# Optimization experiments

Hardware: AMD Instinct MI355X
Metric: run time of the kernel (lower is better)

The kernel has to match this reference:

```python
import jax, jax.numpy as jnp
import numpy as np

B, T, D, VQ, L2, HID = 8, 2048, 768, 64, 12, 1024
K = 2 ** L2          # 4096 codebook entries
N_MID = 4            # condition_layer=6 -> 1 input + 4 middle + 1 output Linear, 5 BatchNorms
EPS_N = 1e-6
EPS_BN = 1e-5


def setup_inputs() -> dict:
    key = jax.random.key(0)
    ks = jax.random.split(key, 10)
    g = lambda i, shape, sc: jax.random.normal(ks[i], shape, jnp.float32) * sc
    return {
        "h_in": jax.random.normal(ks[0], (B, D, T), jnp.float32),
        "attn_mask": jax.random.randint(ks[1], (B, T), 0, 2, jnp.int32),
        "proj_w": g(2, (VQ, D), 0.02), "proj_b": jnp.zeros((VQ,), jnp.float32),
        "inv_w": g(3, (D, VQ), 0.02), "inv_b": jnp.zeros((D,), jnp.float32),
        "mlp_w_in": g(4, (HID, L2), 0.1), "mlp_b_in": jnp.zeros((HID,), jnp.float32),
        "mlp_w_mid": g(5, (N_MID, HID, HID), 0.03), "mlp_b_mid": jnp.zeros((N_MID, HID), jnp.float32),
        "mlp_w_out": g(6, (VQ, HID), 0.03), "mlp_b_out": jnp.zeros((VQ,), jnp.float32),
        "bn_gamma": jnp.ones((N_MID + 1, HID), jnp.float32),
        "bn_beta": jnp.zeros((N_MID + 1, HID), jnp.float32),
    }


def _bn(x, gamma, beta):
    # BatchNorm1d, training mode: batch mean / biased var over codebook rows
    m = x.mean(axis=0)
    v = x.var(axis=0)
    return (x - m) * jax.lax.rsqrt(v + EPS_BN) * gamma + beta


def _l2norm(x):
    return x / (jnp.linalg.norm(x, axis=-1, keepdims=True) + EPS_N)


def reference(h_in, attn_mask, proj_w, proj_b, inv_w, inv_b,
              mlp_w_in, mlp_b_in, mlp_w_mid, mlp_b_mid, mlp_w_out, mlp_b_out,
              bn_gamma, bn_beta):
    # --- codebook: binary vectors -> condition MLP (Linear+BN+ReLU x5, Linear) ---
    ints = jnp.arange(K)
    bits = ((ints[:, None] & (1 << jnp.arange(L2 - 1, -1, -1))) > 0).astype(jnp.float32)  # [K, L2]
    x = jax.nn.relu(_bn(bits @ mlp_w_in.T + mlp_b_in, bn_gamma[0], bn_beta[0]))
    for i in range(N_MID):
        x = jax.nn.relu(_bn(x @ mlp_w_mid[i].T + mlp_b_mid[i], bn_gamma[i + 1], bn_beta[i + 1]))
    embed = x @ mlp_w_out.T + mlp_b_out          # [K, VQ]
    embed = _l2norm(embed)                        # sphere=True

    # --- project hidden states: h_in [B,D,T] -> [B,T,VQ] ---
    h = jnp.einsum('bdt,vd->btv', h_in, proj_w) + proj_b
    h = _l2norm(h)

    # --- pairwise squared distances to codebook, argmax of -d (== softmax argmax) ---
    hf = h.reshape(-1, VQ)                                       # [B*T, VQ]
    d = (hf ** 2).sum(-1, keepdims=True) + (embed ** 2).sum(-1) - 2.0 * (hf @ embed.T)  # [B*T, K]
    code = jnp.argmax(-d, axis=-1)                               # [B*T]

    # --- masked gather/scatter quantization (eval path: hard codes) ---
    mask = (attn_mask == 1)                                      # [B, T]
    h_vq = embed[code].reshape(B, T, VQ) * mask[..., None].astype(h.dtype)
    quantized = jnp.einsum('btv,dv->btd', h_vq, inv_w) + inv_b   # proj_inv -> [B, T, D]
    vq_code = jnp.where(mask, code.reshape(B, T), 0)
    return quantized, vq_code
```

## Files before the change

kernel.cpp:

```cpp
#include <hip/hip_runtime.h>
#include <stddef.h>

#define BB   8
#define TT_  2048
#define DD   768
#define VQ_  64
#define L2C  12
#define HID_ 1024
#define KK   4096
#define NMID 4
#define NT   (BB*TT_)

typedef _Float16 h8v __attribute__((ext_vector_type(8)));
typedef float    f4v __attribute__((ext_vector_type(4)));

#define LDA 40

__global__ __launch_bounds__(256) void k_mlp_in(const float* __restrict__ w_in,
                                                const float* __restrict__ b_in,
                                                float* __restrict__ X) {
    __shared__ float ws_[256 * 12];
    __shared__ float bs_[256];
    int tid = threadIdx.x;
    int h0  = blockIdx.x * 256;
    for (int i = tid; i < 256 * 12; i += 256) ws_[i] = w_in[h0 * 12 + i];
    bs_[tid] = b_in[h0 + tid];
    __syncthreads();
    float w[12];
#pragma unroll
    for (int l = 0; l < 12; l++) w[l] = ws_[tid * 12 + l];
    float bias = bs_[tid];
    int k0 = blockIdx.y * 16;
    for (int kk = 0; kk < 16; kk++) {
        int k = k0 + kk;
        float acc = bias;
#pragma unroll
        for (int l = 0; l < 12; l++)
            if ((k >> (11 - l)) & 1) acc += w[l];
        X[(size_t)k * HID_ + h0 + tid] = acc;
    }
}

__global__ __launch_bounds__(256) void k_bn_stats1(const float* __restrict__ Y,
                                                   float* __restrict__ part) {
    int b = blockIdx.x, t = threadIdx.x;
    const float* src = Y + ((size_t)b << 6) * HID_ + (t << 2);
    float sx = 0.f, sy = 0.f, sz = 0.f, sw = 0.f;
    float qx = 0.f, qy = 0.f, qz = 0.f, qw = 0.f;
    for (int r = 0; r < 64; r++) {
        float4 v = *(const float4*)(src + ((size_t)r << 10));
        sx += v.x; sy += v.y; sz += v.z; sw += v.w;
        qx += v.x * v.x; qy += v.y * v.y; qz += v.z * v.z; qw += v.w * v.w;
    }
    *(float4*)(part + ((size_t)b << 10) + (t << 2)) = make_float4(sx, sy, sz, sw);
    *(float4*)(part + 65536 + ((size_t)b << 10) + (t << 2)) = make_float4(qx, qy, qz, qw);
}

__global__ __launch_bounds__(256) void k_bn_stats2(const float* __restrict__ part,
                                                   float* __restrict__ mv) {
    int c = blockIdx.x * 256 + threadIdx.x;
    float s = 0.f, q = 0.f;
    for (int b = 0; b < 64; b++) {
        s += part[((size_t)b << 10) + c];
        q += part[65536 + ((size_t)b << 10) + c];
    }
    float m = s * (1.f / KK);
    float v = q * (1.f / KK) - m * m;
    mv[c] = m; mv[HID_ + c] = v;
}

__global__ __launch_bounds__(256) void k_bn_apply_split(const float* __restrict__ Y,
                                                        const float* __restrict__ mv,
                                                        const float* __restrict__ gamma,
                                                        const float* __restrict__ beta,
                                                        _Float16* __restrict__ Xhi,
                                                        _Float16* __restrict__ Xlo) {
    int i = blockIdx.x * 256 + threadIdx.x;
    int c = (i << 2) & (HID_ - 1);
    float4 x = ((const float4*)Y)[i];
    float4 m = *(const float4*)(mv + c);
    float4 v = *(const float4*)(mv + HID_ + c);
    float4 g = *(const float4*)(gamma + c);
    float4 b = *(const float4*)(beta + c);
    float o[4];
    o[0] = fmaxf(0.f, (x.x - m.x) * (1.f / sqrtf(v.x + 1e-5f)) * g.x + b.x);
    o[1] = fmaxf(0.f, (x.y - m.y) * (1.f / sqrtf(v.y + 1e-5f)) * g.y + b.y);
    o[2] = fmaxf(0.f, (x.z - m.z) * (1.f / sqrtf(v.z + 1e-5f)) * g.z + b.z);
    o[3] = fmaxf(0.f, (x.w - m.w) * (1.f / sqrtf(v.w + 1e-5f)) * g.w + b.w);
    union { _Float16 h[4]; uint2 u; } uh, ul;
#pragma unroll
    for (int j = 0; j < 4; j++) {
        _Float16 h = (_Float16)o[j];
        uh.h[j] = h;
        ul.h[j] = (_Float16)(o[j] - (float)h);
    }
    *(uint2*)(Xhi + ((size_t)i << 2)) = uh.u;
    *(uint2*)(Xlo + ((size_t)i << 2)) = ul.u;
}

__global__ __launch_bounds__(256) void k_gemm_mfma(const _Float16* __restrict__ Ahi,
                                                   const _Float16* __restrict__ Alo,
                                                   const float* __restrict__ W,
                                                   const float* __restrict__ bias,
                                                   float* __restrict__ C,
                                                   int M, int N, int Kd) {
    __shared__ _Float16 sAh[128 * LDA];
    __shared__ _Float16 sAl[128 * LDA];
    __shared__ _Float16 sWh[64 * LDA];
    __shared__ _Float16 sWl[64 * LDA];
    const int tid = threadIdx.x;
    const int m0 = blockIdx.x * 128, n0 = blockIdx.y * 64;
    const int wave = tid >> 6, lane = tid & 63;
    const int wm = (wave >> 1) << 6;
    const int wn = (wave & 1) << 5;
    const int l15 = lane & 15, quad = lane >> 4;

    const int ar = tid >> 1;
    const int ak = (tid & 1) << 4;
    const int wr = tid >> 2;
    const int wk = (tid & 3) << 3;

    f4v acc[4][2];
#pragma unroll
    for (int i = 0; i < 4; i++)
#pragma unroll
        for (int j = 0; j < 2; j++) acc[i][j] = (f4v){0.f, 0.f, 0.f, 0.f};

    const size_t abase = (size_t)(m0 + ar) * Kd + ak;
    const size_t wbase = (size_t)(n0 + wr) * Kd + wk;

    for (int k0 = 0; k0 < Kd; k0 += 32) {
        uint4 a0 = *(const uint4*)(Ahi + abase + k0);
        uint4 a1 = *(const uint4*)(Ahi + abase + k0 + 8);
        uint4 c0 = *(const uint4*)(Alo + abase + k0);
        uint4 c1 = *(const uint4*)(Alo + abase + k0 + 8);
        float4 w0 = *(const float4*)(W + wbase + k0);
        float4 w1 = *(const float4*)(W + wbase + k0 + 4);
        union { _Float16 h[8]; uint4 u; } wh, wl;
        float wf[8] = {w0.x, w0.y, w0.z, w0.w, w1.x, w1.y, w1.z, w1.w};
#pragma unroll
        for (int j = 0; j < 8; j++) {
            _Float16 h = (_Float16)wf[j];
            wh.h[j] = h;
            wl.h[j] = (_Float16)(wf[j] - (float)h);
        }
        __syncthreads();
        *(uint4*)(sAh + ar * LDA + ak)     = a0;
        *(uint4*)(sAh + ar * LDA + ak + 8) = a1;
        *(uint4*)(sAl + ar * LDA + ak)     = c0;
        *(uint4*)(sAl + ar * LDA + ak + 8) = c1;
        *(uint4*)(sWh + wr * LDA + wk) = wh.u;
        *(uint4*)(sWl + wr * LDA + wk) = wl.u;
        __syncthreads();

        h8v ah[4], alv[4], bh[2], bl[2];
#pragma unroll
        for (int i = 0; i < 4; i++) {
            ah[i]  = *(const h8v*)(sAh + (wm + (i << 4) + l15) * LDA + (quad << 3));
            alv[i] = *(const h8v*)(sAl + (wm + (i << 4) + l15) * LDA + (quad << 3));
        }
#pragma unroll
        for (int j = 0; j < 2; j++) {
            bh[j] = *(const h8v*)(sWh + (wn + (j << 4) + l15) * LDA + (quad << 3));
            bl[j] = *(const h8v*)(sWl + (wn + (j << 4) + l15) * LDA + (quad << 3));
        }
#pragma unroll
        for (int i = 0; i < 4; i++)
#pragma unroll
            for (int j = 0; j < 2; j++) {
                acc[i][j] = __builtin_amdgcn_mfma_f32_16x16x32_f16(ah[i],  bh[j], acc[i][j], 0, 0, 0);
                acc[i][j] = __builtin_amdgcn_mfma_f32_16x16x32_f16(ah[i],  bl[j], acc[i][j], 0, 0, 0);
                acc[i][j] = __builtin_amdgcn_mfma_f32_16x16x32_f16(alv[i], bh[j], acc[i][j], 0, 0, 0);
            }
    }
#pragma unroll
    for (int j = 0; j < 2; j++) {
        int col = n0 + wn + (j << 4) + l15;
        float bv = bias[col];
#pragma unroll
        for (int i = 0; i < 4; i++) {
            int row = m0 + wm + (i << 4) + (quad << 2);
#pragma unroll
            for (int r = 0; r < 4; r++)
                C[(size_t)(row + r) * N + col] = acc[i][j][r] + bv;
        }
    }
}

__global__ __launch_bounds__(256) void k_l2norm(float* __restrict__ E,
                                                float* __restrict__ eqh,
                                                _Float16* __restrict__ Ehi,
                                                _Float16* __restrict__ Elo) {
    int tid = threadIdx.x;
    int row = blockIdx.x * 4 + (tid >> 6);
    int v = tid & 63;
    size_t off = ((size_t)row << 6) + v;
    float x = E[off];
    float ss = x * x;
#pragma unroll
    for (int o = 32; o; o >>= 1) ss += __shfl_xor(ss, o, 64);
    float inv = 1.f / (sqrtf(ss) + 1e-6f);
    float xn = x * inv;
    E[off] = xn;
    _Float16 hh = (_Float16)xn;
    Ehi[off] = hh;
    Elo[off] = (_Float16)(xn - (float)hh);
    if (v == 0) eqh[row] = -0.5f * (ss * inv * inv);
}

__global__ __launch_bounds__(256) void k_wsplit(const float* __restrict__ pw,
                                                _Float16* __restrict__ pwhi,
                                                _Float16* __restrict__ pwlo) {
    int i = blockIdx.x * 256 + threadIdx.x;
    float4 w = ((const float4*)pw)[i];
    float wf[4] = {w.x, w.y, w.z, w.w};
    union { _Float16 h[4]; uint2 u; } uh, ul;
#pragma unroll
    for (int j = 0; j < 4; j++) {
        _Float16 h = (_Float16)wf[j];
        uh.h[j] = h;
        ul.h[j] = (_Float16)(wf[j] - (float)h);
    }
    *(uint2*)(pwhi + ((size_t)i << 2)) = uh.u;
    *(uint2*)(pwlo + ((size_t)i << 2)) = ul.u;
}

__global__ __launch_bounds__(256) void k_proj_mfma(const float* __restrict__ h_in,
                                                   const _Float16* __restrict__ pwhi,
                                                   const _Float16* __restrict__ pwlo,
                                                   float* __restrict__ Hpart) {
    __shared__ float shA[128 * 33];
    const int tid = threadIdx.x;
    const int t0 = blockIdx.x * 128;
    const int ks = blockIdx.y;
    const int b = t0 >> 11;
    const int tloc0 = t0 & (TT_ - 1);
    const int wave = tid >> 6, lane = tid & 63;
    const int l15 = lane & 15, quad = lane >> 4;

    const int dl = tid >> 3;
    const int tg = (tid & 7) << 4;

    f4v acc[2][4];
#pragma unroll
    for (int i = 0; i < 2; i++)
#pragma unroll
        for (int j = 0; j < 4; j++) acc[i][j] = (f4v){0.f, 0.f, 0.f, 0.f};

    for (int kk = 0; kk < 6; kk++) {
        int dd0 = ks * 192 + kk * 32;
        const float* src = h_in + ((size_t)(b * DD + dd0 + dl) << 11) + tloc0 + tg;
        float4 g0 = *(const float4*)(src);
        float4 g1 = *(const float4*)(src + 4);
        float4 g2 = *(const float4*)(src + 8);
        float4 g3 = *(const float4*)(src + 12);
        __syncthreads();
        float gv[16] = {g0.x, g0.y, g0.z, g0.w, g1.x, g1.y, g1.z, g1.w,
                        g2.x, g2.y, g2.z, g2.w, g3.x, g3.y, g3.z, g3.w};
#pragma unroll
        for (int i = 0; i < 16; i++) shA[(tg + i) * 33 + dl] = gv[i];
        __syncthreads();

        h8v ah[2], al[2];
#pragma unroll
        for (int mt = 0; mt < 2; mt++) {
            const float* ap = &shA[((wave << 5) + (mt << 4) + l15) * 33 + (quad << 3)];
            float4 a0 = *(const float4*)(ap);
            float4 a1 = *(const float4*)(ap + 4);
            float av[8] = {a0.x, a0.y, a0.z, a0.w, a1.x, a1.y, a1.z, a1.w};
#pragma unroll
            for (int j = 0; j < 8; j++) {
                _Float16 h = (_Float16)av[j];
                ah[mt][j] = h;
                al[mt][j] = (_Float16)(av[j] - (float)h);
            }
        }
#pragma unroll
        for (int nt = 0; nt < 4; nt++) {
            size_t wb = (size_t)((nt << 4) + l15) * DD + dd0 + (quad << 3);
            h8v bh = *(const h8v*)(pwhi + wb);
            h8v bl = *(const h8v*)(pwlo + wb);
#pragma unroll
            for (int mt = 0; mt < 2; mt++) {
                acc[mt][nt] = __builtin_amdgcn_mfma_f32_16x16x32_f16(ah[mt], bh, acc[mt][nt], 0, 0, 0);
                acc[mt][nt] = __builtin_amdgcn_mfma_f32_16x16x32_f16(ah[mt], bl, acc[mt][nt], 0, 0, 0);
                acc[mt][nt] = __builtin_amdgcn_mfma_f32_16x16x32_f16(al[mt], bh, acc[mt][nt], 0, 0, 0);
            }
        }
    }
    float* dst = Hpart + ((size_t)ks << 20);
#pragma unroll
    for (int mt = 0; mt < 2; mt++) {
#pragma unroll
        for (int r = 0; r < 4; r++) {
            int t = t0 + (wave << 5) + (mt << 4) + (quad << 2) + r;
#pragma unroll
            for (int nt = 0; nt < 4; nt++)
                dst[((size_t)t << 6) + (nt << 4) + l15] = acc[mt][nt][r];
        }
    }
}

__global__ __launch_bounds__(256) void k_hnorm(const float* __restrict__ Hpart,
                                               const float* __restrict__ pb,
                                               _Float16* __restrict__ Hhi,
                                               _Float16* __restrict__ Hlo) {
    __shared__ float ssp[4][64];
    int tid = threadIdx.x;
    int tt = tid & 63, vg = tid >> 6;
    int t = blockIdx.x * 64 + tt;
    size_t base = ((size_t)t << 6) + (vg << 4);
    float o[16];
#pragma unroll
    for (int u = 0; u < 4; u++) {
        float4 p0 = *(const float4*)(Hpart + (0u << 20) + base + (u << 2));
        float4 p1 = *(const float4*)(Hpart + (1u << 20) + base + (u << 2));
        float4 p2 = *(const float4*)(Hpart + (2u << 20) + base + (u << 2));
        float4 p3 = *(const float4*)(Hpart + (3u << 20) + base + (u << 2));
        o[u * 4 + 0] = p0.x + p1.x + p2.x + p3.x;
        o[u * 4 + 1] = p0.y + p1.y + p2.y + p3.y;
        o[u * 4 + 2] = p0.z + p1.z + p2.z + p3.z;
        o[u * 4 + 3] = p0.w + p1.w + p2.w + p3.w;
    }
    float sp = 0.f;
#pragma unroll
    for (int j = 0; j < 16; j++) {
        o[j] += pb[(vg << 4) + j];
        sp = fmaf(o[j], o[j], sp);
    }
    ssp[vg][tt] = sp;
    __syncthreads();
    float ss = ssp[0][tt] + ssp[1][tt] + ssp[2][tt] + ssp[3][tt];
    float inv = 1.f / (sqrtf(ss) + 1e-6f);
    union { _Float16 h[8]; uint4 u; } uh0, uh1, ul0, ul1;
#pragma unroll
    for (int j = 0; j < 16; j++) {
        float xn = o[j] * inv;
        _Float16 hh = (_Float16)xn;
        _Float16 ll = (_Float16)(xn - (float)hh);
        if (j < 8) { uh0.h[j] = hh; ul0.h[j] = ll; }
        else       { uh1.h[j - 8] = hh; ul1.h[j - 8] = ll; }
    }
    *(uint4*)(Hhi + base)     = uh0.u;
    *(uint4*)(Hhi + base + 8) = uh1.u;
    *(uint4*)(Hlo + base)     = ul0.u;
    *(uint4*)(Hlo + base + 8) = ul1.u;
}

__global__ __launch_bounds__(256) void k_argmax_mfma(const _Float16* __restrict__ Hhi,
                                                     const _Float16* __restrict__ Hlo,
                                                     const _Float16* __restrict__ Ehi,
                                                     const _Float16* __restrict__ Elo,
                                                     const float* __restrict__ eqh,
                                                     float* __restrict__ ps,
                                                     int* __restrict__ pi) {
    int tid = threadIdx.x;
    int wave = tid >> 6, lane = tid & 63;
    int l15 = lane & 15, quad = lane >> 4;
    int t0 = blockIdx.x * 256 + wave * 64;
    int kh = blockIdx.y;
    const int kbase = kh << 9;

    h8v hh0[4], hh1[4], hl0[4], hl1[4];
#pragma unroll
    for (int s = 0; s < 4; s++) {
        size_t hb = (size_t)(t0 + (s << 4) + l15) * 64 + (quad << 3);
        hh0[s] = *(const h8v*)(Hhi + hb);
        hh1[s] = *(const h8v*)(Hhi + hb + 32);
        hl0[s] = *(const h8v*)(Hlo + hb);
        hl1[s] = *(const h8v*)(Hlo + hb + 32);
    }
    float best[4] = {-1e30f, -1e30f, -1e30f, -1e30f};
    int   idx[4]  = {0, 0, 0, 0};

    size_t eb = (size_t)(kbase + l15) * 64 + (quad << 3);
    h8v eh0 = *(const h8v*)(Ehi + eb);
    h8v eh1 = *(const h8v*)(Ehi + eb + 32);
    h8v el0 = *(const h8v*)(Elo + eb);
    h8v el1 = *(const h8v*)(Elo + eb + 32);
    float4 q4 = *(const float4*)(eqh + kbase + (quad << 2));

    for (int it = 0; it < 32; it++) {
        h8v ce0 = eh0, ce1 = eh1, cl0 = el0, cl1 = el1;
        float4 cq = q4;
        int k0 = kbase + (it << 4);
        int kn = k0 + 16;
        if (kn > KK - 16) kn = KK - 16;
        size_t ebn = (size_t)(kn + l15) * 64 + (quad << 3);
        eh0 = *(const h8v*)(Ehi + ebn);
        eh1 = *(const h8v*)(Ehi + ebn + 32);
        el0 = *(const h8v*)(Elo + ebn);
        el1 = *(const h8v*)(Elo + ebn + 32);
        q4 = *(const float4*)(eqh + kn + (quad << 2));

        f4v acc[4];
#pragma unroll
        for (int s = 0; s < 4; s++) acc[s] = (f4v){0.f, 0.f, 0.f, 0.f};
#pragma unroll
        for (int s = 0; s < 4; s++) acc[s] = __builtin_amdgcn_mfma_f32_16x16x32_f16(ce0, hh0[s], acc[s], 0, 0, 0);
#pragma unroll
        for (int s = 0; s < 4; s++) acc[s] = __builtin_amdgcn_mfma_f32_16x16x32_f16(ce1, hh1[s], acc[s], 0, 0, 0);
#pragma unroll
        for (int s = 0; s < 4; s++) acc[s] = __builtin_amdgcn_mfma_f32_16x16x32_f16(cl0, hh0[s], acc[s], 0, 0, 0);
#pragma unroll
        for (int s = 0; s < 4; s++) acc[s] = __builtin_amdgcn_mfma_f32_16x16x32_f16(cl1, hh1[s], acc[s], 0, 0, 0);
#pragma unroll
        for (int s = 0; s < 4; s++) acc[s] = __builtin_amdgcn_mfma_f32_16x16x32_f16(ce0, hl0[s], acc[s], 0, 0, 0);
#pragma unroll
        for (int s = 0; s < 4; s++) acc[s] = __builtin_amdgcn_mfma_f32_16x16x32_f16(ce1, hl1[s], acc[s], 0, 0, 0);
        float qv[4] = {cq.x, cq.y, cq.z, cq.w};
#pragma unroll
        for (int r = 0; r < 4; r++) {
            int k = k0 + (quad << 2) + r;
#pragma unroll
            for (int s = 0; s < 4; s++) {
                float sc = acc[s][r] + qv[r];
                if (sc > best[s]) { best[s] = sc; idx[s] = k; }
            }
        }
    }
#pragma unroll
    for (int m = 16; m <= 32; m <<= 1) {
#pragma unroll
        for (int s = 0; s < 4; s++) {
            float ob = __shfl_xor(best[s], m, 64);
            int   oi = __shfl_xor(idx[s], m, 64);
            if (ob > best[s] || (ob == best[s] && oi < idx[s])) { best[s] = ob; idx[s] = oi; }
        }
    }
    if (quad == 0) {
#pragma unroll
        for (int s = 0; s < 4; s++) {
            int t = t0 + (s << 4) + l15;
            ps[(size_t)t * 8 + kh] = best[s];
            pi[(size_t)t * 8 + kh] = idx[s];
        }
    }
}

__global__ __launch_bounds__(256) void k_merge(const float* __restrict__ ps,
                                               const int* __restrict__ pi,
                                               const int* __restrict__ mask,
                                               const float* __restrict__ E,
                                               float* __restrict__ G,
                                               float* __restrict__ outc) {
    __shared__ int codes[256];
    __shared__ int ms[256];
    int tid = threadIdx.x;
    int base = blockIdx.x << 8;
    int t = base + tid;
    float best = ps[(size_t)t * 8];
    int bi = pi[(size_t)t * 8];
#pragma unroll
    for (int s = 1; s < 8; s++) {
        float v = ps[(size_t)t * 8 + s];
        if (v > best) { best = v; bi = pi[(size_t)t * 8 + s]; }
    }
    int m = mask[t];
    codes[tid] = bi;
    ms[tid] = m;
    outc[t] = m ? (float)bi : 0.0f;
    __syncthreads();
    for (int i = tid; i < 256 * 16; i += 256) {
        int r = i >> 4, u = i & 15;
        float4 e = ms[r] ? ((const float4*)(E + ((size_t)codes[r] << 6)))[u]
                         : make_float4(0.f, 0.f, 0.f, 0.f);
        ((float4*)(G + ((size_t)(base + r) << 6)))[u] = e;
    }
}

__global__ __launch_bounds__(256) void k_gemm(const float* __restrict__ A,
                                              const float* __restrict__ W,
                                              const float* __restrict__ bias,
                                              float* __restrict__ C,
                                              int M, int N, int Kd) {
    __shared__ float As[16][68];
    __shared__ float Bs[16][68];
    int tid = threadIdx.x;
    int m0 = blockIdx.x * 64, n0 = blockIdx.y * 64;
    int lr = tid >> 2;
    int lk = (tid & 3) << 2;
    int tx = tid & 15, ty = tid >> 4;
    float acc[4][4] = {};
    for (int k0 = 0; k0 < Kd; k0 += 16) {
        float4 av = *(const float4*)(A + (size_t)(m0 + lr) * Kd + k0 + lk);
        float4 wv = *(const float4*)(W + (size_t)(n0 + lr) * Kd + k0 + lk);
        __syncthreads();
        As[lk + 0][lr] = av.x; As[lk + 1][lr] = av.y;
        As[lk + 2][lr] = av.z; As[lk + 3][lr] = av.w;
        Bs[lk + 0][lr] = wv.x; Bs[lk + 1][lr] = wv.y;
        Bs[lk + 2][lr] = wv.z; Bs[lk + 3][lr] = wv.w;
        __syncthreads();
#pragma unroll
        for (int k = 0; k < 16; k++) {
            const float4 a4 = *(const float4*)&As[k][ty << 2];
            const float4 b4 = *(const float4*)&Bs[k][tx << 2];
            float a[4] = {a4.x, a4.y, a4.z, a4.w};
            float b[4] = {b4.x, b4.y, b4.z, b4.w};
#pragma unroll
            for (int i = 0; i < 4; i++)
#pragma unroll
                for (int j = 0; j < 4; j++)
                    acc[i][j] = fmaf(a[i], b[j], acc[i][j]);
        }
    }
    float bv[4];
#pragma unroll
    for (int j = 0; j < 4; j++) bv[j] = bias[n0 + (tx << 2) + j];
#pragma unroll
    for (int i = 0; i < 4; i++) {
        size_t off = (size_t)(m0 + (ty << 2) + i) * N + n0 + (tx << 2);
        *(float4*)(C + off) =
            make_float4(acc[i][0] + bv[0], acc[i][1] + bv[1],
                        acc[i][2] + bv[2], acc[i][3] + bv[3]);
    }
}

extern "C" void kernel_launch(void* const* d_in, const int* in_sizes, int n_in,
                              void* d_out, int out_size, void* d_ws, size_t ws_size,
                              hipStream_t stream) {
    const float* h_in   = (const float*)d_in[0];
    const int*   amask  = (const int*)d_in[1];
    const float* proj_w = (const float*)d_in[2];
    const float* proj_b = (const float*)d_in[3];
    const float* inv_w  = (const float*)d_in[4];
    const float* inv_b  = (const float*)d_in[5];
    const float* w_in   = (const float*)d_in[6];
    const float* b_in   = (const float*)d_in[7];
    const float* w_mid  = (const float*)d_in[8];
    const float* b_mid  = (const float*)d_in[9];
    const float* w_out  = (const float*)d_in[10];
    const float* b_out  = (const float*)d_in[11];
    const float* gamma  = (const float*)d_in[12];
    const float* beta   = (const float*)d_in[13];

    float*     Y    = (float*)d_ws;
    _Float16*  Xhi  = (_Float16*)(Y + (size_t)KK * HID_);
    _Float16*  Xlo  = Xhi + (size_t)KK * HID_;
    float*     mv   = (float*)(Xlo + (size_t)KK * HID_);
    float*     Emb  = mv + 2 * HID_;
    float*     eqh  = Emb + (size_t)KK * VQ_;
    float*     spart= eqh + KK;
    _Float16*  pwhi = (_Float16*)(spart + 2 * 65536);
    _Float16*  pwlo = pwhi + (size_t)VQ_ * DD;
    float*    Hpart = Y;
    _Float16* H16hi = Xhi;
    _Float16* H16lo = H16hi + (size_t)NT * VQ_;
    _Float16* E16hi = H16lo + (size_t)NT * VQ_;
    _Float16* E16lo = E16hi + (size_t)KK * VQ_;
    float*    ps    = (float*)(E16lo + (size_t)KK * VQ_);
    int*      pidx  = (int*)(ps + (size_t)NT * 8);
    float*    G     = (float*)(pidx + (size_t)NT * 8);

    float* out_q = (float*)d_out;
    float* out_c = out_q + (size_t)NT * DD;

    k_mlp_in<<<dim3(HID_ / 256, KK / 16), 256, 0, stream>>>(w_in, b_in, Y);
    k_bn_stats1<<<64, 256, 0, stream>>>(Y, spart);
    k_bn_stats2<<<4, 256, 0, stream>>>(spart, mv);
    k_bn_apply_split<<<KK * HID_ / 1024, 256, 0, stream>>>(Y, mv, gamma, beta, Xhi, Xlo);
    for (int i = 0; i < NMID; i++) {
        k_gemm_mfma<<<dim3(KK / 128, HID_ / 64), 256, 0, stream>>>(
            Xhi, Xlo, w_mid + (size_t)i * HID_ * HID_, b_mid + (size_t)i * HID_, Y,
            KK, HID_, HID_);
        k_bn_stats1<<<64, 256, 0, stream>>>(Y, spart);
        k_bn_stats2<<<4, 256, 0, stream>>>(spart, mv);
        k_bn_apply_split<<<KK * HID_ / 1024, 256, 0, stream>>>(Y, mv,
            gamma + (size_t)(i + 1) * HID_, beta + (size_t)(i + 1) * HID_, Xhi, Xlo);
    }
    k_gemm_mfma<<<dim3(KK / 128, VQ_ / 64), 256, 0, stream>>>(
        Xhi, Xlo, w_out, b_out, Emb, KK, VQ_, HID_);
    k_l2norm<<<KK / 4, 256, 0, stream>>>(Emb, eqh, E16hi, E16lo);

    k_wsplit<<<VQ_ * DD / 1024, 256, 0, stream>>>(proj_w, pwhi, pwlo);
    k_proj_mfma<<<dim3(NT / 128, 4), 256, 0, stream>>>(h_in, pwhi, pwlo, Hpart);
    k_hnorm<<<NT / 64, 256, 0, stream>>>(Hpart, proj_b, H16hi, H16lo);
    k_argmax_mfma<<<dim3(NT / 256, 8), 256, 0, stream>>>(
        H16hi, H16lo, E16hi, E16lo, eqh, ps, pidx);
    k_merge<<<NT / 256, 256, 0, stream>>>(ps, pidx, amask, Emb, G, out_c);
    k_gemm<<<dim3(NT / 64, DD / 64), 256, 0, stream>>>(
        G, inv_w, inv_b, out_q, NT, DD, VQ_);
}
```

Measured before the change: 539.8 us.

## Use fp16 MFMA for output projection, split argmax wider, widen BN stats grid

The final inverse projection, previously an FP32 SIMT GEMM, now runs on fp16 MFMA. The gathered codebook rows are stored as fp16 (hi part only) and inv_w is converted to fp16 by a new kernel. The argmax kernel splits the codebook into 16 chunks instead of 8 to double grid parallelism, and k_merge reduces 16 partials. BN stats pass 1 uses a 2D grid with scalar loads for more blocks. Dropping the lo part of the embedding and fp16 weights reduces precision of the quantized output.

```diff
diff --git a/kernel.cpp b/kernel.cpp
--- a/kernel.cpp
+++ b/kernel.cpp
@@ -43,17 +43,16 @@
 
 __global__ __launch_bounds__(256) void k_bn_stats1(const float* __restrict__ Y,
                                                    float* __restrict__ part) {
-    int b = blockIdx.x, t = threadIdx.x;
-    const float* src = Y + ((size_t)b << 6) * HID_ + (t << 2);
-    float sx = 0.f, sy = 0.f, sz = 0.f, sw = 0.f;
-    float qx = 0.f, qy = 0.f, qz = 0.f, qw = 0.f;
+    int b = blockIdx.x;
+    int c = blockIdx.y * 256 + threadIdx.x;
+    const float* src = Y + ((size_t)b << 6) * HID_ + c;
+    float s = 0.f, q = 0.f;
     for (int r = 0; r < 64; r++) {
-        float4 v = *(const float4*)(src + ((size_t)r << 10));
-        sx += v.x; sy += v.y; sz += v.z; sw += v.w;
-        qx += v.x * v.x; qy += v.y * v.y; qz += v.z * v.z; qw += v.w * v.w;
-    }
-    *(float4*)(part + ((size_t)b << 10) + (t << 2)) = make_float4(sx, sy, sz, sw);
-    *(float4*)(part + 65536 + ((size_t)b << 10) + (t << 2)) = make_float4(qx, qy, qz, qw);
+        float v = src[(size_t)r << 10];
+        s += v; q += v * v;
+    }
+    part[((size_t)b << 10) + c] = s;
+    part[65536 + ((size_t)b << 10) + c] = q;
 }
 
 __global__ __launch_bounds__(256) void k_bn_stats2(const float* __restrict__ part,
@@ -225,6 +224,16 @@
     *(uint2*)(pwlo + ((size_t)i << 2)) = ul.u;
 }
 
+__global__ __launch_bounds__(256) void k_cvt_inv(const float* __restrict__ iw,
+                                                 _Float16* __restrict__ iwh) {
+    int i = blockIdx.x * 256 + threadIdx.x;
+    float4 w = ((const float4*)iw)[i];
+    union { _Float16 h[4]; uint2 u; } uh;
+    uh.h[0] = (_Float16)w.x; uh.h[1] = (_Float16)w.y;
+    uh.h[2] = (_Float16)w.z; uh.h[3] = (_Float16)w.w;
+    *(uint2*)(iwh + ((size_t)i << 2)) = uh.u;
+}
+
 __global__ __launch_bounds__(256) void k_proj_mfma(const float* __restrict__ h_in,
                                                    const _Float16* __restrict__ pwhi,
                                                    const _Float16* __restrict__ pwlo,
@@ -359,7 +368,7 @@
     int l15 = lane & 15, quad = lane >> 4;
     int t0 = blockIdx.x * 256 + wave * 64;
     int kh = blockIdx.y;
-    const int kbase = kh << 9;
+    const int kbase = kh << 8;
 
     h8v hh0[4], hh1[4], hl0[4], hl1[4];
 #pragma unroll
@@ -380,7 +389,7 @@
     h8v el1 = *(const h8v*)(Elo + eb + 32);
     float4 q4 = *(const float4*)(eqh + kbase + (quad << 2));
 
-    for (int it = 0; it < 32; it++) {
+    for (int it = 0; it < 16; it++) {
         h8v ce0 = eh0, ce1 = eh1, cl0 = el0, cl1 = el1;
         float4 cq = q4;
         int k0 = kbase + (it << 4);
@@ -432,8 +441,8 @@
 #pragma unroll
         for (int s = 0; s < 4; s++) {
             int t = t0 + (s << 4) + l15;
-            ps[(size_t)t * 8 + kh] = best[s];
-            pi[(size_t)t * 8 + kh] = idx[s];
+            ps[(size_t)t * 16 + kh] = best[s];
+            pi[(size_t)t * 16 + kh] = idx[s];
         }
     }
 }
@@ -441,78 +450,76 @@
 __global__ __launch_bounds__(256) void k_merge(const float* __restrict__ ps,
                                                const int* __restrict__ pi,
                                                const int* __restrict__ mask,
-                                               const float* __restrict__ E,
-                                               float* __restrict__ G,
+                                               const _Float16* __restrict__ Ehi,
+                                               _Float16* __restrict__ G16,
                                                float* __restrict__ outc) {
     __shared__ int codes[256];
     __shared__ int ms[256];
     int tid = threadIdx.x;
     int base = blockIdx.x << 8;
     int t = base + tid;
-    float best = ps[(size_t)t * 8];
-    int bi = pi[(size_t)t * 8];
-#pragma unroll
-    for (int s = 1; s < 8; s++) {
-        float v = ps[(size_t)t * 8 + s];
-        if (v > best) { best = v; bi = pi[(size_t)t * 8 + s]; }
+    float best = ps[(size_t)t * 16];
+    int bi = pi[(size_t)t * 16];
+#pragma unroll
+    for (int s = 1; s < 16; s++) {
+        float v = ps[(size_t)t * 16 + s];
+        if (v > best) { best = v; bi = pi[(size_t)t * 16 + s]; }
     }
     int m = mask[t];
     codes[tid] = bi;
     ms[tid] = m;
     outc[t] = m ? (float)bi : 0.0f;
     __syncthreads();
-    for (int i = tid; i < 256 * 16; i += 256) {
-        int r = i >> 4, u = i & 15;
-        float4 e = ms[r] ? ((const float4*)(E + ((size_t)codes[r] << 6)))[u]
-                         : make_float4(0.f, 0.f, 0.f, 0.f);
-        ((float4*)(G + ((size_t)(base + r) << 6)))[u] = e;
-    }
-}
-
-__global__ __launch_bounds__(256) void k_gemm(const float* __restrict__ A,
-                                              const float* __restrict__ W,
-                                              const float* __restrict__ bias,
-                                              float* __restrict__ C,
-                                              int M, int N, int Kd) {
-    __shared__ float As[16][68];
-    __shared__ float Bs[16][68];
-    int tid = threadIdx.x;
-    int m0 = blockIdx.x * 64, n0 = blockIdx.y * 64;
-    int lr = tid >> 2;
-    int lk = (tid & 3) << 2;
-    int tx = tid & 15, ty = tid >> 4;
-    float acc[4][4] = {};
-    for (int k0 = 0; k0 < Kd; k0 += 16) {
-        float4 av = *(const float4*)(A + (size_t)(m0 + lr) * Kd + k0 + lk);
-        float4 wv = *(const float4*)(W + (size_t)(n0 + lr) * Kd + k0 + lk);
-        __syncthreads();
-        As[lk + 0][lr] = av.x; As[lk + 1][lr] = av.y;
-        As[lk + 2][lr] = av.z; As[lk + 3][lr] = av.w;
-        Bs[lk + 0][lr] = wv.x; Bs[lk + 1][lr] = wv.y;
-        Bs[lk + 2][lr] = wv.z; Bs[lk + 3][lr] = wv.w;
-        __syncthreads();
-#pragma unroll
-        for (int k = 0; k < 16; k++) {
-            const float4 a4 = *(const float4*)&As[k][ty << 2];
-            const float4 b4 = *(const float4*)&Bs[k][tx << 2];
-            float a[4] = {a4.x, a4.y, a4.z, a4.w};
-            float b[4] = {b4.x, b4.y, b4.z, b4.w};
-#pragma unroll
-            for (int i = 0; i < 4; i++)
-#pragma unroll
-                for (int j = 0; j < 4; j++)
-                    acc[i][j] = fmaf(a[i], b[j], acc[i][j]);
-        }
-    }
-    float bv[4];
-#pragma unroll
-    for (int j = 0; j < 4; j++) bv[j] = bias[n0 + (tx << 2) + j];
-#pragma unroll
-    for (int i = 0; i < 4; i++) {
-        size_t off = (size_t)(m0 + (ty << 2) + i) * N + n0 + (tx << 2);
-        *(float4*)(C + off) =
-            make_float4(acc[i][0] + bv[0], acc[i][1] + bv[1],
-                        acc[i][2] + bv[2], acc[i][3] + bv[3]);
+    for (int i = tid; i < 256 * 8; i += 256) {
+        int r = i >> 3, u = i & 7;
+        uint4 e = ms[r] ? ((const uint4*)(Ehi + ((size_t)codes[r] << 6)))[u]
+                        : make_uint4(0u, 0u, 0u, 0u);
+        ((uint4*)(G16 + ((size_t)(base + r) << 6)))[u] = e;
+    }
+}
+
+__global__ __launch_bounds__(256) void k_gemm_out(const _Float16* __restrict__ G16,
+                                                  const _Float16* __restrict__ iwh,
+                                                  const float* __restrict__ bias,
+                                                  float* __restrict__ C) {
+    const int tid = threadIdx.x;
+    const int t0 = blockIdx.x * 128, n0 = blockIdx.y * 64;
+    const int wave = tid >> 6, lane = tid & 63;
+    const int l15 = lane & 15, quad = lane >> 4;
+
+    f4v acc[2][4];
+#pragma unroll
+    for (int i = 0; i < 2; i++)
+#pragma unroll
+        for (int j = 0; j < 4; j++) acc[i][j] = (f4v){0.f, 0.f, 0.f, 0.f};
+
+#pragma unroll
+    for (int ks = 0; ks < 2; ks++) {
+        int kk = (ks << 5) + (quad << 3);
+        h8v a[2], b[4];
+#pragma unroll
+        for (int mt = 0; mt < 2; mt++)
+            a[mt] = *(const h8v*)(G16 + (size_t)(t0 + (wave << 5) + (mt << 4) + l15) * 64 + kk);
+#pragma unroll
+        for (int nt = 0; nt < 4; nt++)
+            b[nt] = *(const h8v*)(iwh + (size_t)(n0 + (nt << 4) + l15) * 64 + kk);
+#pragma unroll
+        for (int mt = 0; mt < 2; mt++)
+#pragma unroll
+            for (int nt = 0; nt < 4; nt++)
+                acc[mt][nt] = __builtin_amdgcn_mfma_f32_16x16x32_f16(a[mt], b[nt], acc[mt][nt], 0, 0, 0);
+    }
+#pragma unroll
+    for (int nt = 0; nt < 4; nt++) {
+        int col = n0 + (nt << 4) + l15;
+        float bv = bias[col];
+#pragma unroll
+        for (int mt = 0; mt < 2; mt++) {
+            int row = t0 + (wave << 5) + (mt << 4) + (quad << 2);
+#pragma unroll
+            for (int r = 0; r < 4; r++)
+                C[(size_t)(row + r) * DD + col] = acc[mt][nt][r] + bv;
+        }
     }
 }
 
@@ -549,21 +556,22 @@
     _Float16* E16hi = H16lo + (size_t)NT * VQ_;
     _Float16* E16lo = E16hi + (size_t)KK * VQ_;
     float*    ps    = (float*)(E16lo + (size_t)KK * VQ_);
-    int*      pidx  = (int*)(ps + (size_t)NT * 8);
-    float*    G     = (float*)(pidx + (size_t)NT * 8);
+    int*      pidx  = (int*)(ps + (size_t)NT * 16);
+    _Float16* G16   = (_Float16*)(pidx + (size_t)NT * 16);
+    _Float16* iwh   = G16 + (size_t)NT * VQ_;
 
     float* out_q = (float*)d_out;
     float* out_c = out_q + (size_t)NT * DD;
 
     k_mlp_in<<<dim3(HID_ / 256, KK / 16), 256, 0, stream>>>(w_in, b_in, Y);
-    k_bn_stats1<<<64, 256, 0, stream>>>(Y, spart);
+    k_bn_stats1<<<dim3(64, 4), 256, 0, stream>>>(Y, spart);
     k_bn_stats2<<<4, 256, 0, stream>>>(spart, mv);
     k_bn_apply_split<<<KK * HID_ / 1024, 256, 0, stream>>>(Y, mv, gamma, beta, Xhi, Xlo);
     for (int i = 0; i < NMID; i++) {
         k_gemm_mfma<<<dim3(KK / 128, HID_ / 64), 256, 0, stream>>>(
             Xhi, Xlo, w_mid + (size_t)i * HID_ * HID_, b_mid + (size_t)i * HID_, Y,
             KK, HID_, HID_);
-        k_bn_stats1<<<64, 256, 0, stream>>>(Y, spart);
+        k_bn_stats1<<<dim3(64, 4), 256, 0, stream>>>(Y, spart);
         k_bn_stats2<<<4, 256, 0, stream>>>(spart, mv);
         k_bn_apply_split<<<KK * HID_ / 1024, 256, 0, stream>>>(Y, mv,
             gamma + (size_t)(i + 1) * HID_, beta + (size_t)(i + 1) * HID_, Xhi, Xlo);
@@ -573,11 +581,11 @@
     k_l2norm<<<KK / 4, 256, 0, stream>>>(Emb, eqh, E16hi, E16lo);
 
     k_wsplit<<<VQ_ * DD / 1024, 256, 0, stream>>>(proj_w, pwhi, pwlo);
+    k_cvt_inv<<<VQ_ * DD / 1024, 256, 0, stream>>>(inv_w, iwh);
     k_proj_mfma<<<dim3(NT / 128, 4), 256, 0, stream>>>(h_in, pwhi, pwlo, Hpart);
     k_hnorm<<<NT / 64, 256, 0, stream>>>(Hpart, proj_b, H16hi, H16lo);
-    k_argmax_mfma<<<dim3(NT / 256, 8), 256, 0, stream>>>(
+    k_argmax_mfma<<<dim3(NT / 256, 16), 256, 0, stream>>>(
         H16hi, H16lo, E16hi, E16lo, eqh, ps, pidx);
-    k_merge<<<NT / 256, 256, 0, stream>>>(ps, pidx, amask, Emb, G, out_c);
-    k_gemm<<<dim3(NT / 64, DD / 64), 256, 0, stream>>>(
-        G, inv_w, inv_b, out_q, NT, DD, VQ_);
-}
+    k_merge<<<NT / 256, 256, 0, stream>>>(ps, pidx, amask, E16hi, G16, out_c);
+    k_gemm_out<<<dim3(NT / 128, DD / 64), 256, 0, stream>>>(G16, iwh, inv_b, out_q);
+}
```

After: 515.1 us. 4.6% less time.
